# Kernel optimization log

Measured on AMD Instinct MI355X. Metric: run time of the kernel, lower is better.

Reference implementation:

```python
import jax, jax.numpy as jnp
import numpy as np

B, S, H = 16, 4096, 768
N_SENT = 32
HH = H // 2  # per-direction LSTM hidden
NUM_LAYERS = 2


def attn_pool(x, mask, Wp, bp, v):
    # x: [N, L, H]; torch Linear is x @ W.T + b
    scores = jnp.einsum('nlh,h->nl', jnp.tanh(jnp.einsum('nlh,gh->nlg', x, Wp) + bp), v)
    if mask is not None:
        scores = jnp.where(mask, scores, -jnp.inf)
    w = jax.nn.softmax(scores, axis=1)  # [N, L]
    pooled = jnp.einsum('nlh,nl->nh', x, w)
    return pooled, w


def lstm_dir(x, Wih, Whh, bih, bhh, reverse):
    # x: [B, T, In]; PyTorch gate order i, f, g, o
    xg = jnp.einsum('bti,gi->btg', x, Wih) + bih  # [B, T, 4*HH]
    Bn = x.shape[0]
    init = (jnp.zeros((Bn, HH), x.dtype), jnp.zeros((Bn, HH), x.dtype))

    def step(carry, xt):
        h, c = carry
        g = xt + jnp.einsum('bh,gh->bg', h, Whh) + bhh
        i, f, gg, o = jnp.split(g, 4, axis=-1)
        c = jax.nn.sigmoid(f) * c + jax.nn.sigmoid(i) * jnp.tanh(gg)
        h = jax.nn.sigmoid(o) * jnp.tanh(c)
        return (h, c), h

    _, hs = jax.lax.scan(step, init, jnp.swapaxes(xg, 0, 1), reverse=reverse)
    return jnp.swapaxes(hs, 0, 1)  # [B, T, HH], time-aligned


def bilstm(x, Wih, Whh, bih, bhh):
    h = x
    for l in range(NUM_LAYERS):
        f = lstm_dir(h, Wih[l, 0], Whh[l, 0], bih[l, 0], bhh[l, 0], False)
        b = lstm_dir(h, Wih[l, 1], Whh[l, 1], bih[l, 1], bhh[l, 1], True)
        h = jnp.concatenate([f, b], axis=-1)  # [B, T, H]
    return h


def setup_inputs() -> dict:
    key = jax.random.key(0)
    ks = jax.random.split(key, 12)
    std = 0.02
    return {
        'hidden_states': jax.random.normal(ks[0], (B, S, H), jnp.float32),
        'attention_mask': jnp.ones((B, S), jnp.bool_),
        'w_proj_w': jax.random.normal(ks[1], (H, H), jnp.float32) * std,
        'w_proj_b': jnp.zeros((H,), jnp.float32),
        'w_vec': jax.random.normal(ks[2], (H,), jnp.float32) * std,
        'lstm_Wih': jax.random.normal(ks[3], (NUM_LAYERS, 2, 4 * HH, H), jnp.float32) * std,
        'lstm_Whh': jax.random.normal(ks[4], (NUM_LAYERS, 2, 4 * HH, HH), jnp.float32) * std,
        'lstm_bih': jnp.zeros((NUM_LAYERS, 2, 4 * HH), jnp.float32),
        'lstm_bhh': jnp.zeros((NUM_LAYERS, 2, 4 * HH), jnp.float32),
        's_proj_w': jax.random.normal(ks[5], (H, H), jnp.float32) * std,
        's_proj_b': jnp.zeros((H,), jnp.float32),
        's_vec': jax.random.normal(ks[6], (H,), jnp.float32) * std,
        'n_sent': N_SENT,
    }


def reference(hidden_states, attention_mask, w_proj_w, w_proj_b, w_vec,
              lstm_Wih, lstm_Whh, lstm_bih, lstm_bhh,
              s_proj_w, s_proj_b, s_vec, n_sent):
    b, s, h = hidden_states.shape
    L = s // n_sent
    # uniform sentence segmentation (boundaries at k*L-1): vectorized word attention
    x = hidden_states.reshape(b * n_sent, L, h)
    m = attention_mask.reshape(b * n_sent, L)
    pooled, w_attn = attn_pool(x, m, w_proj_w, w_proj_b, w_vec)  # [b*n_sent, h]
    sent = pooled.reshape(b, n_sent, h)
    enc = bilstm(sent, lstm_Wih, lstm_Whh, lstm_bih, lstm_bhh)  # [b, n_sent, h]
    doc, s_attn = attn_pool(enc, None, s_proj_w, s_proj_b, s_vec)  # [b, h]
    return doc, w_attn.reshape(b, n_sent, L), s_attn
```

## Files before the change

kernel.cpp:

```cpp
#include <hip/hip_runtime.h>
#include <math.h>

#define NB     16
#define NSENT  32
#define LW     128
#define HD     768
#define HH     384
#define NG     1536
#define NROWS  (NB*NSENT)
#define MW     (NROWS*LW)

typedef unsigned short ushort_t;
typedef unsigned long long u64;
typedef __attribute__((ext_vector_type(8))) short bf16x8;
typedef __attribute__((ext_vector_type(4))) float f32x4;
typedef __attribute__((ext_vector_type(4))) unsigned short u16x4;
typedef __attribute__((ext_vector_type(4))) unsigned int u32x4;

#define MFMA_BF16(a, b, c) __builtin_amdgcn_mfma_f32_16x16x32_bf16((a), (b), (c), 0, 0, 0)

__device__ __forceinline__ ushort_t f2bf(float x) {
  union { float f; unsigned u; } v; v.f = x;
  unsigned r = v.u + 0x7FFFu + ((v.u >> 16) & 1u);
  return (ushort_t)(r >> 16);
}
__device__ __forceinline__ float tanh_fast(float x) {
  float e = __builtin_amdgcn_exp2f(x * 2.88539008177793f);
  return 1.0f - 2.0f * __builtin_amdgcn_rcpf(e + 1.0f);
}
__device__ __forceinline__ float sigm(float x) {
  float e = __builtin_amdgcn_exp2f(-x * 1.44269504088896f);
  return __builtin_amdgcn_rcpf(1.0f + e);
}
__device__ __forceinline__ bf16x8 cvt8(float4 x, float4 y) {
  union { unsigned u[4]; bf16x8 v; } o;
  asm("v_cvt_pk_bf16_f32 %0, %1, %2" : "=v"(o.u[0]) : "v"(x.x), "v"(x.y));
  asm("v_cvt_pk_bf16_f32 %0, %1, %2" : "=v"(o.u[1]) : "v"(x.z), "v"(x.w));
  asm("v_cvt_pk_bf16_f32 %0, %1, %2" : "=v"(o.u[2]) : "v"(y.x), "v"(y.y));
  asm("v_cvt_pk_bf16_f32 %0, %1, %2" : "=v"(o.u[3]) : "v"(y.z), "v"(y.w));
  return o.v;
}
__device__ __forceinline__ u64 ld64_ic(const u64* p) {
  return __hip_atomic_load(p, __ATOMIC_RELAXED, __HIP_MEMORY_SCOPE_AGENT);
}
__device__ __forceinline__ void st32_ic(unsigned* p, unsigned v) {
  __hip_atomic_store(p, v, __ATOMIC_RELAXED, __HIP_MEMORY_SCOPE_AGENT);
}
__device__ __forceinline__ bool bad64(u64 v) {
  return ((unsigned)v == 0xFFFFFFFFu) | ((unsigned)(v >> 32) == 0xFFFFFFFFu);
}

__global__ void cvt_kernel(const float* __restrict__ in, ushort_t* __restrict__ out, int n) {
  int i = blockIdx.x * blockDim.x + threadIdx.x;
  int st = gridDim.x * blockDim.x;
  for (; i < n; i += st) out[i] = f2bf(in[i]);
}

__global__ void addvec_kernel(const float* __restrict__ a, const float* __restrict__ b,
                              float* __restrict__ o, int n) {
  int i = blockIdx.x * blockDim.x + threadIdx.x;
  if (i < n) o[i] = a[i] + b[i];
}

__global__ void fillu_kernel(unsigned* __restrict__ p, unsigned v, int n) {
  int i = blockIdx.x * blockDim.x + threadIdx.x;
  int st = gridDim.x * blockDim.x;
  for (; i < n; i += st) p[i] = v;
}

template<int MODE, int SWZ>
__global__ __launch_bounds__(512, 2) void gemm_kernel(
    const float* __restrict__ Af, const ushort_t* __restrict__ Ab,
    const ushort_t* __restrict__ W, const float* __restrict__ bias,
    const float* __restrict__ vvec, float* __restrict__ outp,
    int Mtotal, int Ntot)
{
  __shared__ __align__(16) char smem[81920];
  short* Albuf = (short*)smem;
  short* Blbuf = (short*)(smem + 32768);
  float* pbuf  = (float*)smem;

  const int tid = threadIdx.x;
  int nc, m0;
  if constexpr (SWZ == 1) {
    const int g = blockIdx.x;
    const int x = g & 7, s = g >> 3;
    nc = s & 3;
    m0 = (x + 8 * (s >> 2)) * 128;
  } else {
    nc = blockIdx.x;
    m0 = blockIdx.y * 128;
  }
  const int n0 = nc * 192;

  const int rowA = tid >> 3, uA = tid & 7;
  const unsigned ubase = (unsigned)(uA ^ (rowA & 7));
  const unsigned soff = (unsigned)((rowA * 8 + ubase) * 16);

  const int w = tid >> 6, wr = w >> 2, wc = w & 3;
  const int l = tid & 63, lm = l & 15, lg = l >> 4;
  int arow[4], ar7[4];
  #pragma unroll
  for (int mt = 0; mt < 4; ++mt) { arow[mt] = wr * 64 + mt * 16 + lm; ar7[mt] = arow[mt] & 7; }
  int brow[3], br7[3];
  #pragma unroll
  for (int nt = 0; nt < 3; ++nt) { brow[nt] = wc * 48 + nt * 16 + lm; br7[nt] = brow[nt] & 7; }

  f32x4 acc[4][3];
  #pragma unroll
  for (int mt = 0; mt < 4; ++mt)
    #pragma unroll
    for (int nt = 0; nt < 3; ++nt) acc[mt][nt] = (f32x4){0.f, 0.f, 0.f, 0.f};

  float4 a4[4]; bf16x8 a8[2]; bf16x8 b8[3];

  auto issue = [&](int s) {
    const int kc = s * 64 + uA * 8;
    if constexpr (MODE == 0) {
      const float* ap = Af + (size_t)(m0 + rowA) * HD + kc;
      a4[0] = *(const float4*)(ap);
      a4[1] = *(const float4*)(ap + 4);
      a4[2] = *(const float4*)(ap + (size_t)64 * HD);
      a4[3] = *(const float4*)(ap + (size_t)64 * HD + 4);
    } else {
      const ushort_t* ap = Ab + (size_t)(m0 + rowA) * HD + kc;
      a8[0] = *(const bf16x8*)(ap);
      a8[1] = *(const bf16x8*)(ap + (size_t)64 * HD);
    }
    #pragma unroll
    for (int i = 0; i < 3; ++i)
      b8[i] = *(const bf16x8*)(W + (size_t)(n0 + rowA + 64 * i) * HD + kc);
  };
  auto commit = [&](int buf) {
    short* Ad = Albuf + buf * 8192;
    short* Bd = Blbuf + buf * 12288;
    bf16x8 w0, w1;
    if constexpr (MODE == 0) { w0 = cvt8(a4[0], a4[1]); w1 = cvt8(a4[2], a4[3]); }
    else                     { w0 = a8[0];              w1 = a8[1]; }
    *(bf16x8*)((char*)Ad + soff) = w0;
    *(bf16x8*)((char*)Ad + soff + 8192) = w1;
    #pragma unroll
    for (int i = 0; i < 3; ++i)
      *(bf16x8*)((char*)Bd + soff + (unsigned)i * 8192) = b8[i];
  };

  issue(0);
  commit(0);
  int cur = 0;
  for (int s = 0; s < 12; ++s) {
    __syncthreads();
    if (s < 11) issue(s + 1);
    const short* Asrc = Albuf + cur * 8192;
    const short* Bsrc = Blbuf + cur * 12288;
    #pragma unroll
    for (int kk = 0; kk < 2; ++kk) {
      const int u = kk * 4 + lg;
      bf16x8 af[4], bfr[3];
      #pragma unroll
      for (int mt = 0; mt < 4; ++mt)
        af[mt] = *(const bf16x8*)((const char*)Asrc + (unsigned)((arow[mt] * 8 + (u ^ ar7[mt])) << 4));
      #pragma unroll
      for (int nt = 0; nt < 3; ++nt)
        bfr[nt] = *(const bf16x8*)((const char*)Bsrc + (unsigned)((brow[nt] * 8 + (u ^ br7[nt])) << 4));
      #pragma unroll
      for (int mt = 0; mt < 4; ++mt)
        #pragma unroll
        for (int nt = 0; nt < 3; ++nt)
          acc[mt][nt] = MFMA_BF16(af[mt], bfr[nt], acc[mt][nt]);
    }
    if (s < 11) commit(cur ^ 1);
    cur ^= 1;
  }

  if constexpr (MODE == 0) {
    float sp[16];
    #pragma unroll
    for (int e = 0; e < 16; ++e) sp[e] = 0.f;
    #pragma unroll
    for (int nt = 0; nt < 3; ++nt) {
      const int col = n0 + wc * 48 + nt * 16 + lm;
      const float bb = bias[col], vv = vvec[col];
      #pragma unroll
      for (int mt = 0; mt < 4; ++mt)
        #pragma unroll
        for (int r = 0; r < 4; ++r)
          sp[mt * 4 + r] += tanh_fast(acc[mt][nt][r] + bb) * vv;
    }
    #pragma unroll
    for (int msk = 1; msk < 16; msk <<= 1)
      #pragma unroll
      for (int e = 0; e < 16; ++e) sp[e] += __shfl_xor(sp[e], msk, 64);
    __syncthreads();
    if (lm == 0) {
      #pragma unroll
      for (int mt = 0; mt < 4; ++mt)
        #pragma unroll
        for (int r = 0; r < 4; ++r)
          pbuf[(wr * 4 + wc) * 64 + mt * 16 + lg * 4 + r] = sp[mt * 4 + r];
    }
    __syncthreads();
    if (tid < 128) {
      const int wrr = tid >> 6, idx = tid & 63;
      float ssum = pbuf[(wrr * 4 + 0) * 64 + idx] + pbuf[(wrr * 4 + 1) * 64 + idx]
                 + pbuf[(wrr * 4 + 2) * 64 + idx] + pbuf[(wrr * 4 + 3) * 64 + idx];
      outp[(size_t)nc * Mtotal + m0 + wrr * 64 + idx] = ssum;
    }
  } else {
    #pragma unroll
    for (int nt = 0; nt < 3; ++nt) {
      const int col = n0 + wc * 48 + nt * 16 + lm;
      const float bb = bias[col];
      #pragma unroll
      for (int mt = 0; mt < 4; ++mt) {
        const int mrow = m0 + wr * 64 + mt * 16 + lg * 4;
        #pragma unroll
        for (int r = 0; r < 4; ++r)
          outp[(size_t)(mrow + r) * Ntot + col] = acc[mt][nt][r] + bb;
      }
    }
  }
}

__global__ __launch_bounds__(64) void softmax128_kernel(const float* __restrict__ sc,
                                                        float* __restrict__ wout) {
  const int row = blockIdx.x, lane = threadIdx.x;
  float a = sc[row * 128 + lane]          + sc[MW + row * 128 + lane]
          + sc[2 * MW + row * 128 + lane] + sc[3 * MW + row * 128 + lane];
  float b = sc[row * 128 + 64 + lane]          + sc[MW + row * 128 + 64 + lane]
          + sc[2 * MW + row * 128 + 64 + lane] + sc[3 * MW + row * 128 + 64 + lane];
  float mx = fmaxf(a, b);
  #pragma unroll
  for (int m = 1; m < 64; m <<= 1) mx = fmaxf(mx, __shfl_xor(mx, m, 64));
  float ea = __builtin_amdgcn_exp2f((a - mx) * 1.44269504088896f);
  float eb = __builtin_amdgcn_exp2f((b - mx) * 1.44269504088896f);
  float s = ea + eb;
  #pragma unroll
  for (int m = 1; m < 64; m <<= 1) s += __shfl_xor(s, m, 64);
  float inv = 1.0f / s;
  wout[row * 128 + lane] = ea * inv;
  wout[row * 128 + 64 + lane] = eb * inv;
}

__global__ __launch_bounds__(192) void pool_kernel(
    const float* __restrict__ x, const float* __restrict__ wattn,
    ushort_t* __restrict__ pooledbf)
{
  __shared__ float wl[128];
  const int n = blockIdx.x, tid = threadIdx.x;
  if (tid < 128) wl[tid] = wattn[n * 128 + tid];
  __syncthreads();
  const float* xb = x + (size_t)n * LW * HD + tid * 4;
  float a0 = 0, a1 = 0, a2 = 0, a3 = 0;
  float b0 = 0, b1 = 0, b2 = 0, b3 = 0;
  for (int lq = 0; lq < LW; lq += 2) {
    float4 v0 = *(const float4*)(xb + (size_t)lq * HD);
    float4 v1 = *(const float4*)(xb + (size_t)(lq + 1) * HD);
    float w0 = wl[lq], w1 = wl[lq + 1];
    a0 += w0 * v0.x; a1 += w0 * v0.y; a2 += w0 * v0.z; a3 += w0 * v0.w;
    b0 += w1 * v1.x; b1 += w1 * v1.y; b2 += w1 * v1.z; b3 += w1 * v1.w;
  }
  u16x4 o;
  o[0] = f2bf(a0 + b0); o[1] = f2bf(a1 + b1); o[2] = f2bf(a2 + b2); o[3] = f2bf(a3 + b3);
  *(u16x4*)(pooledbf + (size_t)n * HD + tid * 4) = o;
}

__global__ __launch_bounds__(384) void lstm_kernel(
    const ushort_t* __restrict__ whh_l,
    const float* __restrict__ xg,
    unsigned* __restrict__ hb32,
    ushort_t* __restrict__ encbf,
    float* __restrict__ encf,
    int writef32)
{
  __shared__ __align__(16) short h_lds[16 * HH];
  __shared__ float gatebuf[16][100];
  __shared__ float cst[16][24];
  const int tid = threadIdx.x;
  const int d = blockIdx.x >> 4, cid = blockIdx.x & 15;
  const int w = tid >> 6, l = tid & 63, lm = l & 15, lg = l >> 4;
  const int b = tid / 24, jj = tid % 24, gj = cid * 24 + jj;

  bf16x8 wf[12];
  {
    int r = w * 16 + lm;
    int qq = r / 24, jjr = r % 24;
    const ushort_t* src = whh_l + ((size_t)d * NG + qq * HH + cid * 24 + jjr) * HH + lg * 8;
    #pragma unroll
    for (int kk = 0; kk < 12; ++kk) wf[kk] = *(const bf16x8*)(src + kk * 32);
  }
  cst[b][jj] = 0.f;
  __syncthreads();

  const int hr = tid / 24, hc = tid % 24;
  const int hu = hc * 2, hx = hr & 7;

  for (int t = 0; t < NSENT; ++t) {
    const int trev = d ? (NSENT - 1 - t) : t;
    const float* xp = xg + (size_t)(b * NSENT + trev) * 3072 + d * NG + gj;
    float xi = xp[0], xf = xp[HH], xgg = xp[2 * HH], xo = xp[3 * HH];

    f32x4 acc = (f32x4){0.f, 0.f, 0.f, 0.f};
    if (t > 0) {
      const u64* src = (const u64*)hb32 + (size_t)(d * NSENT + (t - 1)) * 1536 + hr * 96 + hc * 4;
      u64 v0, v1, v2, v3;
      for (;;) {
        v0 = ld64_ic(src + 0); v1 = ld64_ic(src + 1);
        v2 = ld64_ic(src + 2); v3 = ld64_ic(src + 3);
        if (!(bad64(v0) | bad64(v1) | bad64(v2) | bad64(v3))) break;
        __builtin_amdgcn_s_sleep(1);
      }
      u32x4 lo = (u32x4){(unsigned)v0, (unsigned)(v0 >> 32), (unsigned)v1, (unsigned)(v1 >> 32)};
      u32x4 hi = (u32x4){(unsigned)v2, (unsigned)(v2 >> 32), (unsigned)v3, (unsigned)(v3 >> 32)};
      *(u32x4*)((char*)h_lds + (unsigned)((hr * 48 + ((hu    ) ^ hx)) * 16)) = lo;
      *(u32x4*)((char*)h_lds + (unsigned)((hr * 48 + ((hu + 1) ^ hx)) * 16)) = hi;
      __syncthreads();

      #pragma unroll
      for (int kk = 0; kk < 12; ++kk) {
        bf16x8 a = *(const bf16x8*)((char*)h_lds +
                      (unsigned)((lm * 48 + ((kk * 4 + lg) ^ (lm & 7))) * 16));
        acc = MFMA_BF16(a, wf[kk], acc);
      }
    }
    #pragma unroll
    for (int r = 0; r < 4; ++r)
      gatebuf[lg * 4 + r][w * 16 + lm] = acc[r];
    __syncthreads();

    {
      float gi = gatebuf[b][jj]      + xi;
      float gf = gatebuf[b][24 + jj] + xf;
      float gg = gatebuf[b][48 + jj] + xgg;
      float go = gatebuf[b][72 + jj] + xo;
      float c = sigm(gf) * cst[b][jj] + sigm(gi) * tanh_fast(gg);
      float h = sigm(go) * tanh_fast(c);
      cst[b][jj] = c;
      unsigned hv = (unsigned)f2bf(h);
      unsigned up = __shfl_down(hv, 1);
      if ((jj & 1) == 0 && t < NSENT - 1)
        st32_ic(hb32 + (size_t)(d * NSENT + t) * 3072 + b * 192 + gj / 2, hv | (up << 16));
      size_t eo = ((size_t)b * NSENT + trev) * HD + d * HH + gj;
      if (writef32) encf[eo] = h;
      else          encbf[eo] = f2bf(h);
    }
    __syncthreads();
  }
}

__global__ __launch_bounds__(64) void softmax32_kernel(const float* __restrict__ sc,
                                                       float* __restrict__ sattn,
                                                       float* __restrict__ sw) {
  const int b = blockIdx.x, lane = threadIdx.x;
  if (lane >= 32) return;
  float v = sc[b * 32 + lane]              + sc[NROWS + b * 32 + lane]
          + sc[2 * NROWS + b * 32 + lane]  + sc[3 * NROWS + b * 32 + lane];
  float mx = v;
  #pragma unroll
  for (int m = 1; m < 32; m <<= 1) mx = fmaxf(mx, __shfl_xor(mx, m, 32));
  float e = __builtin_amdgcn_exp2f((v - mx) * 1.44269504088896f);
  float s = e;
  #pragma unroll
  for (int m = 1; m < 32; m <<= 1) s += __shfl_xor(s, m, 32);
  float wv = e / s;
  sattn[b * 32 + lane] = wv;
  sw[b * 32 + lane] = wv;
}

__global__ __launch_bounds__(256) void doc_kernel(const float* __restrict__ enc2,
                                                  const float* __restrict__ sw,
                                                  float* __restrict__ doc) {
  __shared__ float wl[32];
  const int b = blockIdx.x, tid = threadIdx.x;
  if (tid < 32) wl[tid] = sw[b * 32 + tid];
  __syncthreads();
  for (int h = tid; h < HD; h += 256) {
    float a = 0.f;
    #pragma unroll
    for (int t = 0; t < 32; ++t) a += wl[t] * enc2[((size_t)b * 32 + t) * HD + h];
    doc[(size_t)b * HD + h] = a;
  }
}

extern "C" void kernel_launch(void* const* d_in, const int* in_sizes, int n_in,
                              void* d_out, int out_size, void* d_ws, size_t ws_size,
                              hipStream_t stream) {
  const float* hs  = (const float*)d_in[0];
  const float* wpw = (const float*)d_in[2];
  const float* wpb = (const float*)d_in[3];
  const float* wv  = (const float*)d_in[4];
  const float* Wih = (const float*)d_in[5];
  const float* Whh = (const float*)d_in[6];
  const float* bih = (const float*)d_in[7];
  const float* bhh = (const float*)d_in[8];
  const float* spw = (const float*)d_in[9];
  const float* spb = (const float*)d_in[10];
  const float* sv  = (const float*)d_in[11];

  float* out   = (float*)d_out;
  float* doc   = out;
  float* wattn = out + NB * HD;
  float* sattn = out + NB * HD + NROWS * LW;

  char* p = (char*)d_ws;
  auto take = [&p](size_t bytes) { char* q = p; p += (bytes + 255) & ~(size_t)255; return q; };
  ushort_t* wp_bf   = (ushort_t*)take((size_t)HD * HD * 2);
  ushort_t* sp_bf   = (ushort_t*)take((size_t)HD * HD * 2);
  ushort_t* wih_bf  = (ushort_t*)take((size_t)4 * NG * HD * 2);
  ushort_t* whh_bf  = (ushort_t*)take((size_t)4 * NG * HH * 2);
  float*    biasc   = (float*)take((size_t)4 * NG * 4);
  float*    wscore4 = (float*)take((size_t)4 * MW * 4);
  ushort_t* pooledbf= (ushort_t*)take((size_t)NROWS * HD * 2);
  float*    xgbuf   = (float*)take((size_t)NROWS * 2 * NG * 4);
  unsigned* hslots  = (unsigned*)take((size_t)2 * 2 * NSENT * 3072 * 4);
  ushort_t* enc1_bf = (ushort_t*)take((size_t)NROWS * HD * 2);
  float*    enc2    = (float*)take((size_t)NROWS * HD * 4);
  float*    sscore4 = (float*)take((size_t)4 * NROWS * 4);
  float*    sw      = (float*)take((size_t)NB * NSENT * 4);

  cvt_kernel<<<512, 256, 0, stream>>>(wpw, wp_bf, HD * HD);
  cvt_kernel<<<512, 256, 0, stream>>>(spw, sp_bf, HD * HD);
  cvt_kernel<<<2048, 256, 0, stream>>>(Wih, wih_bf, 4 * NG * HD);
  cvt_kernel<<<1024, 256, 0, stream>>>(Whh, whh_bf, 4 * NG * HH);
  addvec_kernel<<<24, 256, 0, stream>>>(bih, bhh, biasc, 4 * NG);
  fillu_kernel<<<768, 256, 0, stream>>>(hslots, 0xFFFFFFFFu, 2 * 2 * NSENT * 3072);

  gemm_kernel<0, 1><<<dim3(2048), 512, 0, stream>>>(
      hs, nullptr, wp_bf, wpb, wv, wscore4, MW, HD);
  softmax128_kernel<<<NROWS, 64, 0, stream>>>(wscore4, wattn);
  pool_kernel<<<NROWS, 192, 0, stream>>>(hs, wattn, pooledbf);

  gemm_kernel<1, 0><<<dim3(16, NROWS / 128), 512, 0, stream>>>(
      nullptr, pooledbf, wih_bf, biasc, nullptr, xgbuf, NROWS, 2 * NG);
  {
    const ushort_t* a0 = whh_bf; const float* a1 = xgbuf; unsigned* a2 = hslots;
    ushort_t* a3 = enc1_bf; float* a4 = enc2; int a5 = 0;
    void* args[] = { &a0, &a1, &a2, &a3, &a4, &a5 };
    hipLaunchCooperativeKernel((void*)lstm_kernel, dim3(32), dim3(384), args, 0, stream);
  }
  gemm_kernel<1, 0><<<dim3(16, NROWS / 128), 512, 0, stream>>>(
      nullptr, enc1_bf, wih_bf + (size_t)2 * NG * HD, biasc + 2 * NG,
      nullptr, xgbuf, NROWS, 2 * NG);
  {
    const ushort_t* a0 = whh_bf + (size_t)2 * NG * HH; const float* a1 = xgbuf;
    unsigned* a2 = hslots + (size_t)2 * NSENT * 3072;
    ushort_t* a3 = enc1_bf; float* a4 = enc2; int a5 = 1;
    void* args[] = { &a0, &a1, &a2, &a3, &a4, &a5 };
    hipLaunchCooperativeKernel((void*)lstm_kernel, dim3(32), dim3(384), args, 0, stream);
  }

  gemm_kernel<0, 0><<<dim3(4, NROWS / 128), 512, 0, stream>>>(
      enc2, nullptr, sp_bf, spb, sv, sscore4, NROWS, HD);
  softmax32_kernel<<<NB, 64, 0, stream>>>(sscore4, sattn, sw);
  doc_kernel<<<NB, 256, 0, stream>>>(enc2, sw, doc);
}
```

Before: 357.8 us.

## Pre-convert hidden states to bf16 and stage GEMM tiles via direct global-to-LDS loads

Adds a vectorized kernel that converts the fp32 hidden states to bf16 once; both the word-score GEMM and the pooling kernel then read the bf16 copy. The GEMM drops its register-staged A/B loads (and the in-loop fp32-to-bf16 conversion) in favour of global_load_lds with pre-swizzled source addresses and one barrier per k-step. The second LSTM layer now also writes a bf16 encoder output, so the sentence-score GEMM uses the same bf16 path. The cost is an extra full pass over the large hidden-state tensor and a workspace copy, plus lower precision in the word-level weighted pooling sum.

Result: slower. 387.0 us (+8.2%).

```diff
diff --git a/kernel.cpp b/kernel.cpp
--- a/kernel.cpp
+++ b/kernel.cpp
@@ -24,6 +24,9 @@
   unsigned r = v.u + 0x7FFFu + ((v.u >> 16) & 1u);
   return (ushort_t)(r >> 16);
 }
+__device__ __forceinline__ float bf2f(ushort_t b) {
+  union { unsigned u; float f; } v; v.u = ((unsigned)b) << 16; return v.f;
+}
 __device__ __forceinline__ float tanh_fast(float x) {
   float e = __builtin_amdgcn_exp2f(x * 2.88539008177793f);
   return 1.0f - 2.0f * __builtin_amdgcn_rcpf(e + 1.0f);
@@ -40,6 +43,11 @@
   asm("v_cvt_pk_bf16_f32 %0, %1, %2" : "=v"(o.u[3]) : "v"(y.z), "v"(y.w));
   return o.v;
 }
+__device__ __forceinline__ void gload16(const void* g, void* l) {
+  __builtin_amdgcn_global_load_lds(
+      (const __attribute__((address_space(1))) unsigned int*)g,
+      (__attribute__((address_space(3))) unsigned int*)l, 16, 0, 0);
+}
 __device__ __forceinline__ u64 ld64_ic(const u64* p) {
   return __hip_atomic_load(p, __ATOMIC_RELAXED, __HIP_MEMORY_SCOPE_AGENT);
 }
@@ -56,6 +64,16 @@
   for (; i < n; i += st) out[i] = f2bf(in[i]);
 }
 
+__global__ void cvtv_kernel(const float* __restrict__ in, ushort_t* __restrict__ out, int n8) {
+  int i = blockIdx.x * blockDim.x + threadIdx.x;
+  int st = gridDim.x * blockDim.x;
+  for (; i < n8; i += st) {
+    const float4* p = (const float4*)(in + (size_t)i * 8);
+    float4 a = p[0], b = p[1];
+    *(bf16x8*)(out + (size_t)i * 8) = cvt8(a, b);
+  }
+}
+
 __global__ void addvec_kernel(const float* __restrict__ a, const float* __restrict__ b,
                               float* __restrict__ o, int n) {
   int i = blockIdx.x * blockDim.x + threadIdx.x;
@@ -68,12 +86,11 @@
   for (; i < n; i += st) p[i] = v;
 }
 
-template<int MODE, int SWZ>
+template<int EPI, int SWZ>
 __global__ __launch_bounds__(512, 2) void gemm_kernel(
-    const float* __restrict__ Af, const ushort_t* __restrict__ Ab,
-    const ushort_t* __restrict__ W, const float* __restrict__ bias,
-    const float* __restrict__ vvec, float* __restrict__ outp,
-    int Mtotal, int Ntot)
+    const ushort_t* __restrict__ Ab, const ushort_t* __restrict__ W,
+    const float* __restrict__ bias, const float* __restrict__ vvec,
+    float* __restrict__ outp, int Mtotal, int Ntot)
 {
   __shared__ __align__(16) char smem[81920];
   short* Albuf = (short*)smem;
@@ -93,9 +110,7 @@
   }
   const int n0 = nc * 192;
 
-  const int rowA = tid >> 3, uA = tid & 7;
-  const unsigned ubase = (unsigned)(uA ^ (rowA & 7));
-  const unsigned soff = (unsigned)((rowA * 8 + ubase) * 16);
+  const unsigned wbase = (unsigned)(tid & ~63) * 16;
 
   const int w = tid >> 6, wr = w >> 2, wc = w & 3;
   const int l = tid & 63, lm = l & 15, lg = l >> 4;
@@ -112,46 +127,23 @@
     #pragma unroll
     for (int nt = 0; nt < 3; ++nt) acc[mt][nt] = (f32x4){0.f, 0.f, 0.f, 0.f};
 
-  float4 a4[4]; bf16x8 a8[2]; bf16x8 b8[3];
-
-  auto issue = [&](int s) {
-    const int kc = s * 64 + uA * 8;
-    if constexpr (MODE == 0) {
-      const float* ap = Af + (size_t)(m0 + rowA) * HD + kc;
-      a4[0] = *(const float4*)(ap);
-      a4[1] = *(const float4*)(ap + 4);
-      a4[2] = *(const float4*)(ap + (size_t)64 * HD);
-      a4[3] = *(const float4*)(ap + (size_t)64 * HD + 4);
-    } else {
-      const ushort_t* ap = Ab + (size_t)(m0 + rowA) * HD + kc;
-      a8[0] = *(const bf16x8*)(ap);
-      a8[1] = *(const bf16x8*)(ap + (size_t)64 * HD);
-    }
-    #pragma unroll
-    for (int i = 0; i < 3; ++i)
-      b8[i] = *(const bf16x8*)(W + (size_t)(n0 + rowA + 64 * i) * HD + kc);
+  const int a0r = tid >> 3,          a0u = (tid & 7) ^ (a0r & 7);
+  const int a1r = (tid + 512) >> 3,  a1u = (tid & 7) ^ (a1r & 7);
+  const int b2r = (tid + 1024) >> 3, b2u = (tid & 7) ^ (b2r & 7);
+
+  auto stage = [&](int buf, int s) {
+    const int kc = s * 64;
+    char* Ad = (char*)Albuf + buf * 16384;
+    char* Bd = (char*)Blbuf + buf * 24576;
+    gload16(Ab + (size_t)(m0 + a0r) * HD + kc + a0u * 8, Ad + wbase);
+    gload16(Ab + (size_t)(m0 + a1r) * HD + kc + a1u * 8, Ad + 8192 + wbase);
+    gload16(W + (size_t)(n0 + a0r) * HD + kc + a0u * 8, Bd + wbase);
+    gload16(W + (size_t)(n0 + a1r) * HD + kc + a1u * 8, Bd + 8192 + wbase);
+    gload16(W + (size_t)(n0 + b2r) * HD + kc + b2u * 8, Bd + 16384 + wbase);
   };
-  auto commit = [&](int buf) {
-    short* Ad = Albuf + buf * 8192;
-    short* Bd = Blbuf + buf * 12288;
-    bf16x8 w0, w1;
-    if constexpr (MODE == 0) { w0 = cvt8(a4[0], a4[1]); w1 = cvt8(a4[2], a4[3]); }
-    else                     { w0 = a8[0];              w1 = a8[1]; }
-    *(bf16x8*)((char*)Ad + soff) = w0;
-    *(bf16x8*)((char*)Ad + soff + 8192) = w1;
-    #pragma unroll
-    for (int i = 0; i < 3; ++i)
-      *(bf16x8*)((char*)Bd + soff + (unsigned)i * 8192) = b8[i];
-  };
-
-  issue(0);
-  commit(0);
-  int cur = 0;
-  for (int s = 0; s < 12; ++s) {
-    __syncthreads();
-    if (s < 11) issue(s + 1);
-    const short* Asrc = Albuf + cur * 8192;
-    const short* Bsrc = Blbuf + cur * 12288;
+  auto compute = [&](int buf) {
+    const short* Asrc = Albuf + buf * 8192;
+    const short* Bsrc = Blbuf + buf * 12288;
     #pragma unroll
     for (int kk = 0; kk < 2; ++kk) {
       const int u = kk * 4 + lg;
@@ -168,11 +160,19 @@
         for (int nt = 0; nt < 3; ++nt)
           acc[mt][nt] = MFMA_BF16(af[mt], bfr[nt], acc[mt][nt]);
     }
-    if (s < 11) commit(cur ^ 1);
+  };
+
+  stage(0, 0);
+  __syncthreads();
+  int cur = 0;
+  for (int s = 0; s < 12; ++s) {
+    if (s < 11) stage(cur ^ 1, s + 1);
+    compute(cur);
+    __syncthreads();
     cur ^= 1;
   }
 
-  if constexpr (MODE == 0) {
+  if constexpr (EPI == 0) {
     float sp[16];
     #pragma unroll
     for (int e = 0; e < 16; ++e) sp[e] = 0.f;
@@ -190,7 +190,6 @@
     for (int msk = 1; msk < 16; msk <<= 1)
       #pragma unroll
       for (int e = 0; e < 16; ++e) sp[e] += __shfl_xor(sp[e], msk, 64);
-    __syncthreads();
     if (lm == 0) {
       #pragma unroll
       for (int mt = 0; mt < 4; ++mt)
@@ -242,22 +241,24 @@
 }
 
 __global__ __launch_bounds__(192) void pool_kernel(
-    const float* __restrict__ x, const float* __restrict__ wattn,
+    const ushort_t* __restrict__ xbf, const float* __restrict__ wattn,
     ushort_t* __restrict__ pooledbf)
 {
   __shared__ float wl[128];
   const int n = blockIdx.x, tid = threadIdx.x;
   if (tid < 128) wl[tid] = wattn[n * 128 + tid];
   __syncthreads();
-  const float* xb = x + (size_t)n * LW * HD + tid * 4;
+  const ushort_t* xb = xbf + (size_t)n * LW * HD + tid * 4;
   float a0 = 0, a1 = 0, a2 = 0, a3 = 0;
   float b0 = 0, b1 = 0, b2 = 0, b3 = 0;
   for (int lq = 0; lq < LW; lq += 2) {
-    float4 v0 = *(const float4*)(xb + (size_t)lq * HD);
-    float4 v1 = *(const float4*)(xb + (size_t)(lq + 1) * HD);
+    u16x4 v0 = *(const u16x4*)(xb + (size_t)lq * HD);
+    u16x4 v1 = *(const u16x4*)(xb + (size_t)(lq + 1) * HD);
     float w0 = wl[lq], w1 = wl[lq + 1];
-    a0 += w0 * v0.x; a1 += w0 * v0.y; a2 += w0 * v0.z; a3 += w0 * v0.w;
-    b0 += w1 * v1.x; b1 += w1 * v1.y; b2 += w1 * v1.z; b3 += w1 * v1.w;
+    a0 += w0 * bf2f(v0[0]); a1 += w0 * bf2f(v0[1]);
+    a2 += w0 * bf2f(v0[2]); a3 += w0 * bf2f(v0[3]);
+    b0 += w1 * bf2f(v1[0]); b1 += w1 * bf2f(v1[1]);
+    b2 += w1 * bf2f(v1[2]); b3 += w1 * bf2f(v1[3]);
   }
   u16x4 o;
   o[0] = f2bf(a0 + b0); o[1] = f2bf(a1 + b1); o[2] = f2bf(a2 + b2); o[3] = f2bf(a3 + b3);
@@ -340,8 +341,8 @@
       if ((jj & 1) == 0 && t < NSENT - 1)
         st32_ic(hb32 + (size_t)(d * NSENT + t) * 3072 + b * 192 + gj / 2, hv | (up << 16));
       size_t eo = ((size_t)b * NSENT + trev) * HD + d * HH + gj;
+      encbf[eo] = f2bf(h);
       if (writef32) encf[eo] = h;
-      else          encbf[eo] = f2bf(h);
     }
     __syncthreads();
   }
@@ -413,9 +414,11 @@
   float*    xgbuf   = (float*)take((size_t)NROWS * 2 * NG * 4);
   unsigned* hslots  = (unsigned*)take((size_t)2 * 2 * NSENT * 3072 * 4);
   ushort_t* enc1_bf = (ushort_t*)take((size_t)NROWS * HD * 2);
+  ushort_t* enc2_bf = (ushort_t*)take((size_t)NROWS * HD * 2);
   float*    enc2    = (float*)take((size_t)NROWS * HD * 4);
   float*    sscore4 = (float*)take((size_t)4 * NROWS * 4);
   float*    sw      = (float*)take((size_t)NB * NSENT * 4);
+  ushort_t* hs_bf   = (ushort_t*)take((size_t)MW * HD * 2);
 
   cvt_kernel<<<512, 256, 0, stream>>>(wpw, wp_bf, HD * HD);
   cvt_kernel<<<512, 256, 0, stream>>>(spw, sp_bf, HD * HD);
@@ -423,14 +426,15 @@
   cvt_kernel<<<1024, 256, 0, stream>>>(Whh, whh_bf, 4 * NG * HH);
   addvec_kernel<<<24, 256, 0, stream>>>(bih, bhh, biasc, 4 * NG);
   fillu_kernel<<<768, 256, 0, stream>>>(hslots, 0xFFFFFFFFu, 2 * 2 * NSENT * 3072);
+  cvtv_kernel<<<2048, 256, 0, stream>>>(hs, hs_bf, (int)((size_t)MW * HD / 8));
 
   gemm_kernel<0, 1><<<dim3(2048), 512, 0, stream>>>(
-      hs, nullptr, wp_bf, wpb, wv, wscore4, MW, HD);
+      hs_bf, wp_bf, wpb, wv, wscore4, MW, HD);
   softmax128_kernel<<<NROWS, 64, 0, stream>>>(wscore4, wattn);
-  pool_kernel<<<NROWS, 192, 0, stream>>>(hs, wattn, pooledbf);
+  pool_kernel<<<NROWS, 192, 0, stream>>>(hs_bf, wattn, pooledbf);
 
   gemm_kernel<1, 0><<<dim3(16, NROWS / 128), 512, 0, stream>>>(
-      nullptr, pooledbf, wih_bf, biasc, nullptr, xgbuf, NROWS, 2 * NG);
+      pooledbf, wih_bf, biasc, nullptr, xgbuf, NROWS, 2 * NG);
   {
     const ushort_t* a0 = whh_bf; const float* a1 = xgbuf; unsigned* a2 = hslots;
     ushort_t* a3 = enc1_bf; float* a4 = enc2; int a5 = 0;
@@ -438,18 +442,18 @@
     hipLaunchCooperativeKernel((void*)lstm_kernel, dim3(32), dim3(384), args, 0, stream);
   }
   gemm_kernel<1, 0><<<dim3(16, NROWS / 128), 512, 0, stream>>>(
-      nullptr, enc1_bf, wih_bf + (size_t)2 * NG * HD, biasc + 2 * NG,
-      nullptr, xgbuf, NROWS, 2 * NG);
+      enc1_bf, wih_bf + (size_t)2 * NG * HD, biasc + 2 * NG, nullptr,
+      xgbuf, NROWS, 2 * NG);
   {
     const ushort_t* a0 = whh_bf + (size_t)2 * NG * HH; const float* a1 = xgbuf;
     unsigned* a2 = hslots + (size_t)2 * NSENT * 3072;
-    ushort_t* a3 = enc1_bf; float* a4 = enc2; int a5 = 1;
+    ushort_t* a3 = enc2_bf; float* a4 = enc2; int a5 = 1;
     void* args[] = { &a0, &a1, &a2, &a3, &a4, &a5 };
     hipLaunchCooperativeKernel((void*)lstm_kernel, dim3(32), dim3(384), args, 0, stream);
   }
 
   gemm_kernel<0, 0><<<dim3(4, NROWS / 128), 512, 0, stream>>>(
-      enc2, nullptr, sp_bf, spb, sv, sscore4, NROWS, HD);
+      enc2_bf, sp_bf, spb, sv, sscore4, NROWS, HD);
   softmax32_kernel<<<NB, 64, 0, stream>>>(sscore4, sattn, sw);
   doc_kernel<<<NB, 256, 0, stream>>>(enc2, sw, doc);
 }
```
